# Optimization experiments

Hardware: AMD Instinct MI355X
Metric: run time of the kernel (lower is better)

Reference implementation:

```python
import jax, jax.numpy as jnp
import numpy as np

N_NODES = 100000
N_EDGES = 1600000
IN_C, HID_C, OUT_C = 64, 64, 32


def setup_inputs() -> dict:
    key = jax.random.key(0)
    ks = jax.random.split(key, 6)
    x = jax.random.normal(ks[0], (N_NODES, IN_C), dtype=jnp.float32)
    edge_index = jax.random.randint(ks[1], (2, N_EDGES), 0, N_NODES, dtype=jnp.int64)
    edge_weight = jax.random.uniform(ks[2], (N_EDGES,), dtype=jnp.float32)
    # Glorot-ish init for the two GCNConv weight matrices, zero bias (PyG default)
    W1 = jax.random.normal(ks[3], (IN_C, HID_C), dtype=jnp.float32) / np.sqrt(IN_C)
    b1 = jnp.zeros((HID_C,), dtype=jnp.float32)
    W2 = jax.random.normal(ks[4], (HID_C, OUT_C), dtype=jnp.float32) / np.sqrt(HID_C)
    b2 = jnp.zeros((OUT_C,), dtype=jnp.float32)
    return {"x": x, "edge_index": edge_index, "edge_weight": edge_weight,
            "W1": W1, "b1": b1, "W2": W2, "b2": b2}


def _gcn_conv(x, src, dst, w, W, b):
    """PyG GCNConv: add self-loops (weight 1), symmetric D^-1/2 (A+I) D^-1/2 norm,
    then aggregate transformed features into destination nodes, plus bias."""
    n = x.shape[0]
    loop = jnp.arange(n, dtype=src.dtype)
    s = jnp.concatenate([src, loop])
    d = jnp.concatenate([dst, loop])
    wl = jnp.concatenate([w, jnp.ones((n,), dtype=x.dtype)])
    deg = jax.ops.segment_sum(wl, d, num_segments=n)            # [N]
    dinv = jnp.where(deg > 0, jax.lax.rsqrt(deg), 0.0)
    norm = dinv[s] * wl * dinv[d]                               # [E+N]
    xw = x @ W                                                  # [N, C_out]
    msg = norm[:, None] * xw[s]                                 # gather + scale
    return jax.ops.segment_sum(msg, d, num_segments=n) + b      # scatter-add


def reference(x, edge_index, edge_weight, W1, b1, W2, b2):
    src, dst = edge_index[0], edge_index[1]
    h = _gcn_conv(x, src, dst, edge_weight, W1, b1)
    h = jax.nn.relu(h)
    # dropout(p=0.5, training=self.training): identity in eval mode
    return _gcn_conv(h, src, dst, edge_weight, W2, b2)
```

## Files before the change

kernel.cpp:

```cpp
#include <hip/hip_runtime.h>

#define N_NODES 100000
#define N_EDGES 1600000
#define IN_C 64
#define HID_C 64
#define OUT_C 32

#define NB 391
#define BSHIFT 8
#define BMASK 255
#define SEG_CAP 4864
#define EPB 4096
#define BIN_BLOCKS ((N_EDGES + EPB - 1) / EPB)
#define SMASK 0x1FFFF
#define FIXSCALE 34359738368.0f

__device__ __forceinline__ unsigned int bpack(float a, float b) {
    unsigned int ua = __float_as_uint(a);
    ua += 0x7FFFu + ((ua >> 16) & 1u);
    unsigned int ub = __float_as_uint(b);
    ub += 0x7FFFu + ((ub >> 16) & 1u);
    return (ua >> 16) | (ub & 0xFFFF0000u);
}
__device__ __forceinline__ float2 bup(unsigned int v) {
    return make_float2(__uint_as_float(v << 16), __uint_as_float(v & 0xFFFF0000u));
}


__global__ void __launch_bounds__(256) bin_kernel(const int* __restrict__ src,
                                                  const int* __restrict__ dst,
                                                  const float* __restrict__ w,
                                                  int* __restrict__ gcnt,
                                                  int2* __restrict__ seg) {
    __shared__ int2 recs[EPB];
    __shared__ int meta[EPB];
    __shared__ int hist[NB];
    __shared__ int gbase[NB];
    int tid = threadIdx.x;
    for (int i = tid; i < NB; i += 256) hist[i] = 0;
    __syncthreads();
    int e0 = blockIdx.x * EPB;
    int n = min(EPB, N_EDGES - e0);
    const int4* src4 = (const int4*)(src + e0);
    const int4* dst4 = (const int4*)(dst + e0);
    const float4* w4 = (const float4*)(w + e0);
    int n4 = n >> 2;
    for (int i = tid; i < n4; i += 256) {
        int4 s = src4[i];
        int4 d = dst4[i];
        float4 ww = w4[i];
        int j = i << 2;
#define BIN_ONE(K, SS, DD, WW)                                             \
        {                                                                  \
            int b = (DD) >> BSHIFT;                                        \
            recs[j + K] = make_int2((SS) | (((DD) & BMASK) << 17),         \
                                    __float_as_int(WW));                   \
            int rank = atomicAdd(&hist[b], 1);                             \
            meta[j + K] = b | (rank << 9);                                 \
        }
        BIN_ONE(0, s.x, d.x, ww.x)
        BIN_ONE(1, s.y, d.y, ww.y)
        BIN_ONE(2, s.z, d.z, ww.z)
        BIN_ONE(3, s.w, d.w, ww.w)
#undef BIN_ONE
    }
    __syncthreads();
    for (int b = tid; b < NB; b += 256) {
        int c = hist[b];
        gbase[b] = c ? atomicAdd(&gcnt[b], c) : 0;
    }
    __syncthreads();
    for (int i = tid; i < n; i += 256) {
        int m = meta[i];
        int b = m & 511, rank = m >> 9;
        int pos = gbase[b] + rank;
        if (pos < SEG_CAP) seg[(size_t)b * SEG_CAP + pos] = recs[i];
    }
}


__global__ void __launch_bounds__(256) bsort_kernel(const int* __restrict__ gcnt,
                                                    const int2* __restrict__ seg,
                                                    int2* __restrict__ seg2,
                                                    float* __restrict__ dinv,
                                                    int2* __restrict__ rowRC) {
    __shared__ int2 recs[SEG_CAP];
    __shared__ unsigned long long packed[256];
    __shared__ int meta[SEG_CAP];
    __shared__ int sarr[256];
    __shared__ int ofs0[256];
    int tid = threadIdx.x, b = blockIdx.x;
    int n = min(gcnt[b], SEG_CAP);
    const int2* sp = seg + (size_t)b * SEG_CAP;
    packed[tid] = 0ULL;
    __syncthreads();
    for (int i = tid; i < n; i += 256) {
        int2 r = sp[i];
        recs[i] = r;
        int dl = (r.x >> 17) & BMASK;
        unsigned long long fixw =
            (unsigned long long)(__int_as_float(r.y) * FIXSCALE);
        unsigned long long old = atomicAdd(&packed[dl], (1ULL << 48) | fixw);
        meta[i] = dl | ((int)(old >> 48) << 8);
    }
    __syncthreads();
    unsigned long long p = packed[tid];
    int myc = (int)(p >> 48);
    float degw = (float)((double)(p & ((1ULL << 48) - 1)) * (1.0 / (double)FIXSCALE));
    int node = (b << BSHIFT) + tid;
    if (node < N_NODES) dinv[node] = rsqrtf(1.0f + degw);
    int padc = (myc + 1) & ~1;
    sarr[tid] = padc;
    __syncthreads();
    for (int off = 1; off < 256; off <<= 1) {
        int tmp = (tid >= off) ? sarr[tid - off] : 0;
        __syncthreads();
        sarr[tid] += tmp;
        __syncthreads();
    }
    int excl = sarr[tid] - padc;
    if (node < N_NODES) rowRC[node] = make_int2(b * SEG_CAP + excl, myc);
    ofs0[tid] = excl;
    __syncthreads();
    int2* op = seg2 + (size_t)b * SEG_CAP;
    for (int i = tid; i < n; i += 256) {
        int m = meta[i];
        int dl = m & BMASK, rank = m >> 8;
        op[ofs0[dl] + rank] = recs[i];
    }
}


__global__ void __launch_bounds__(256) gemm1_kernel(const float* __restrict__ X,
                                                    const float* __restrict__ W,
                                                    const float* __restrict__ dinv,
                                                    unsigned int* __restrict__ XWs,
                                                    int nRows) {
    __shared__ float XsT[64][64];
    __shared__ float Ws[64][64];
    int tid = threadIdx.x;
    {
        const float4* Wv = (const float4*)W;
        float4* Wsv = (float4*)&Ws[0][0];
        for (int i = tid; i < 1024; i += 256) Wsv[i] = Wv[i];
    }
    int row0 = blockIdx.x * 64;
    int rmax = nRows - row0;
    for (int i = tid; i < 64 * 16; i += 256) {
        int r = i & 63, kq = i >> 6;
        float4 v = (r < rmax) ? ((const float4*)(X + (size_t)(row0 + r) * IN_C))[kq]
                              : make_float4(0.f, 0.f, 0.f, 0.f);
        XsT[4 * kq + 0][r] = v.x;
        XsT[4 * kq + 1][r] = v.y;
        XsT[4 * kq + 2][r] = v.z;
        XsT[4 * kq + 3][r] = v.w;
    }
    __syncthreads();
    int tr = tid >> 4, tc = tid & 15;
    float acc[4][4] = {};
    float a[4], bb[4];
#pragma unroll 8
    for (int k = 0; k < 64; ++k) {
        *(float4*)a = *(const float4*)&XsT[k][4 * tr];
        *(float4*)bb = *(const float4*)&Ws[k][4 * tc];
#pragma unroll
        for (int i = 0; i < 4; ++i)
#pragma unroll
            for (int j = 0; j < 4; ++j) acc[i][j] += a[i] * bb[j];
    }
#pragma unroll
    for (int i = 0; i < 4; ++i) {
        int rl = 4 * tr + i;
        if (rl < rmax) {
            int row = row0 + rl;
            float di = dinv[row];
            uint2 o;
            o.x = bpack(acc[i][0] * di, acc[i][1] * di);
            o.y = bpack(acc[i][2] * di, acc[i][3] * di);
            ((uint2*)XWs)[(size_t)row * 16 + tc] = o;
        }
    }
}


__global__ void __launch_bounds__(256) agg1_kernel(const int2* __restrict__ rowRC,
                                                   const int2* __restrict__ seg2,
                                                   const unsigned int* __restrict__ XWs,
                                                   const float* __restrict__ dinv,
                                                   const float* __restrict__ b1,
                                                   unsigned int* __restrict__ Hb) {
    int l32 = threadIdx.x & 31;
    int d = blockIdx.x * 8 + (threadIdx.x >> 5);
    if (d >= N_NODES) return;
    float did = dinv[d];
    float2 bv = ((const float2*)b1)[l32];
    float2 s2 = bup(XWs[(size_t)d * 32 + l32]);
    float ax = bv.x + did * s2.x, ay = bv.y + did * s2.y;
    int2 rc = rowRC[d];
    int nc = rc.y;
    const int2* sp = seg2 + rc.x;
    const int4* sp4 = (const int4*)sp;
    int e = 0;
    for (; e + 8 <= nc; e += 8) {
        int4 q0 = sp4[(e >> 1) + 0], q1 = sp4[(e >> 1) + 1];
        int4 q2 = sp4[(e >> 1) + 2], q3 = sp4[(e >> 1) + 3];
        int s0 = q0.x & SMASK, s1 = q0.z & SMASK, s4 = q1.x & SMASK, s5 = q1.z & SMASK;
        int s6 = q2.x & SMASK, s7 = q2.z & SMASK, s8 = q3.x & SMASK, s9 = q3.z & SMASK;
        unsigned int r0 = XWs[(size_t)s0 * 32 + l32];
        unsigned int r1 = XWs[(size_t)s1 * 32 + l32];
        unsigned int r2 = XWs[(size_t)s4 * 32 + l32];
        unsigned int r3 = XWs[(size_t)s5 * 32 + l32];
        unsigned int r4 = XWs[(size_t)s6 * 32 + l32];
        unsigned int r5 = XWs[(size_t)s7 * 32 + l32];
        unsigned int r6 = XWs[(size_t)s8 * 32 + l32];
        unsigned int r7 = XWs[(size_t)s9 * 32 + l32];
        float c0 = __int_as_float(q0.y) * did, c1 = __int_as_float(q0.w) * did;
        float c2 = __int_as_float(q1.y) * did, c3 = __int_as_float(q1.w) * did;
        float c4 = __int_as_float(q2.y) * did, c5 = __int_as_float(q2.w) * did;
        float c6 = __int_as_float(q3.y) * did, c7 = __int_as_float(q3.w) * did;
        float2 v;
        v = bup(r0); ax += c0 * v.x; ay += c0 * v.y;
        v = bup(r1); ax += c1 * v.x; ay += c1 * v.y;
        v = bup(r2); ax += c2 * v.x; ay += c2 * v.y;
        v = bup(r3); ax += c3 * v.x; ay += c3 * v.y;
        v = bup(r4); ax += c4 * v.x; ay += c4 * v.y;
        v = bup(r5); ax += c5 * v.x; ay += c5 * v.y;
        v = bup(r6); ax += c6 * v.x; ay += c6 * v.y;
        v = bup(r7); ax += c7 * v.x; ay += c7 * v.y;
    }
    for (; e + 2 <= nc; e += 2) {
        int4 q = sp4[e >> 1];
        int s0 = q.x & SMASK, s1 = q.z & SMASK;
        unsigned int r0 = XWs[(size_t)s0 * 32 + l32];
        unsigned int r1 = XWs[(size_t)s1 * 32 + l32];
        float c0 = __int_as_float(q.y) * did, c1 = __int_as_float(q.w) * did;
        float2 v;
        v = bup(r0); ax += c0 * v.x; ay += c0 * v.y;
        v = bup(r1); ax += c1 * v.x; ay += c1 * v.y;
    }
    if (e < nc) {
        int2 p = sp[e];
        int s = p.x & SMASK;
        float c = __int_as_float(p.y) * did;
        float2 v = bup(XWs[(size_t)s * 32 + l32]);
        ax += c * v.x;
        ay += c * v.y;
    }
    Hb[(size_t)d * 32 + l32] = bpack(fmaxf(ax, 0.f), fmaxf(ay, 0.f));
}


__global__ void __launch_bounds__(256) gemm2_kernel(const unsigned int* __restrict__ Hb,
                                                    const float* __restrict__ W,
                                                    const float* __restrict__ dinv,
                                                    unsigned int* __restrict__ HWs,
                                                    int nRows) {
    __shared__ float HsT[64][128];
    __shared__ float Ws[64][32];
    int tid = threadIdx.x;
    {
        const float4* Wv = (const float4*)W;
        float4* Wsv = (float4*)&Ws[0][0];
        for (int i = tid; i < 512; i += 256) Wsv[i] = Wv[i];
    }
    int row0 = blockIdx.x * 128;
    int rmax = nRows - row0;
    for (int i = tid; i < 128 * 8; i += 256) {
        int r = i & 127, kq = i >> 7;
        uint4 v = (r < rmax) ? ((const uint4*)(Hb + (size_t)(row0 + r) * 32))[kq]
                             : make_uint4(0u, 0u, 0u, 0u);
        float2 f;
        f = bup(v.x); HsT[8 * kq + 0][r] = f.x; HsT[8 * kq + 1][r] = f.y;
        f = bup(v.y); HsT[8 * kq + 2][r] = f.x; HsT[8 * kq + 3][r] = f.y;
        f = bup(v.z); HsT[8 * kq + 4][r] = f.x; HsT[8 * kq + 5][r] = f.y;
        f = bup(v.w); HsT[8 * kq + 6][r] = f.x; HsT[8 * kq + 7][r] = f.y;
    }
    __syncthreads();
    int tr = tid >> 3, tc = tid & 7;
    float acc[4][4] = {};
    float a[4], bb[4];
#pragma unroll 8
    for (int k = 0; k < 64; ++k) {
        *(float4*)a = *(const float4*)&HsT[k][4 * tr];
        *(float4*)bb = *(const float4*)&Ws[k][4 * tc];
#pragma unroll
        for (int i = 0; i < 4; ++i)
#pragma unroll
            for (int j = 0; j < 4; ++j) acc[i][j] += a[i] * bb[j];
    }
#pragma unroll
    for (int i = 0; i < 4; ++i) {
        int rl = 4 * tr + i;
        if (rl < rmax) {
            int row = row0 + rl;
            float di = dinv[row];
            uint2 o;
            o.x = bpack(acc[i][0] * di, acc[i][1] * di);
            o.y = bpack(acc[i][2] * di, acc[i][3] * di);
            ((uint2*)HWs)[(size_t)row * 8 + tc] = o;
        }
    }
}


__global__ void __launch_bounds__(256) agg2_kernel(const int2* __restrict__ rowRC,
                                                   const int2* __restrict__ seg2,
                                                   const unsigned int* __restrict__ HWs,
                                                   const float* __restrict__ dinv,
                                                   const float* __restrict__ b2,
                                                   float* __restrict__ out) {
    int l16 = threadIdx.x & 15;
    int d = blockIdx.x * 16 + (threadIdx.x >> 4);
    if (d >= N_NODES) return;
    float did = dinv[d];
    float2 bv = ((const float2*)b2)[l16];
    float2 s2 = bup(HWs[(size_t)d * 16 + l16]);
    float ax = bv.x + did * s2.x, ay = bv.y + did * s2.y;
    int2 rc = rowRC[d];
    int nc = rc.y;
    const int2* sp = seg2 + rc.x;
    const int4* sp4 = (const int4*)sp;
    int e = 0;
    for (; e + 8 <= nc; e += 8) {
        int4 q0 = sp4[(e >> 1) + 0], q1 = sp4[(e >> 1) + 1];
        int4 q2 = sp4[(e >> 1) + 2], q3 = sp4[(e >> 1) + 3];
        int s0 = q0.x & SMASK, s1 = q0.z & SMASK, s4 = q1.x & SMASK, s5 = q1.z & SMASK;
        int s6 = q2.x & SMASK, s7 = q2.z & SMASK, s8 = q3.x & SMASK, s9 = q3.z & SMASK;
        unsigned int r0 = HWs[(size_t)s0 * 16 + l16];
        unsigned int r1 = HWs[(size_t)s1 * 16 + l16];
        unsigned int r2 = HWs[(size_t)s4 * 16 + l16];
        unsigned int r3 = HWs[(size_t)s5 * 16 + l16];
        unsigned int r4 = HWs[(size_t)s6 * 16 + l16];
        unsigned int r5 = HWs[(size_t)s7 * 16 + l16];
        unsigned int r6 = HWs[(size_t)s8 * 16 + l16];
        unsigned int r7 = HWs[(size_t)s9 * 16 + l16];
        float c0 = __int_as_float(q0.y) * did, c1 = __int_as_float(q0.w) * did;
        float c2 = __int_as_float(q1.y) * did, c3 = __int_as_float(q1.w) * did;
        float c4 = __int_as_float(q2.y) * did, c5 = __int_as_float(q2.w) * did;
        float c6 = __int_as_float(q3.y) * did, c7 = __int_as_float(q3.w) * did;
        float2 v;
        v = bup(r0); ax += c0 * v.x; ay += c0 * v.y;
        v = bup(r1); ax += c1 * v.x; ay += c1 * v.y;
        v = bup(r2); ax += c2 * v.x; ay += c2 * v.y;
        v = bup(r3); ax += c3 * v.x; ay += c3 * v.y;
        v = bup(r4); ax += c4 * v.x; ay += c4 * v.y;
        v = bup(r5); ax += c5 * v.x; ay += c5 * v.y;
        v = bup(r6); ax += c6 * v.x; ay += c6 * v.y;
        v = bup(r7); ax += c7 * v.x; ay += c7 * v.y;
    }
    for (; e + 2 <= nc; e += 2) {
        int4 q = sp4[e >> 1];
        int s0 = q.x & SMASK, s1 = q.z & SMASK;
        unsigned int r0 = HWs[(size_t)s0 * 16 + l16];
        unsigned int r1 = HWs[(size_t)s1 * 16 + l16];
        float c0 = __int_as_float(q.y) * did, c1 = __int_as_float(q.w) * did;
        float2 v;
        v = bup(r0); ax += c0 * v.x; ay += c0 * v.y;
        v = bup(r1); ax += c1 * v.x; ay += c1 * v.y;
    }
    if (e < nc) {
        int2 p = sp[e];
        int s = p.x & SMASK;
        float c = __int_as_float(p.y) * did;
        float2 v = bup(HWs[(size_t)s * 16 + l16]);
        ax += c * v.x;
        ay += c * v.y;
    }
    ((float2*)out)[(size_t)d * 16 + l16] = make_float2(ax, ay);
}


extern "C" void kernel_launch(void* const* d_in, const int* in_sizes, int n_in,
                              void* d_out, int out_size, void* d_ws, size_t ws_size,
                              hipStream_t stream) {
    const float* x = (const float*)d_in[0];
    const int* edge_index = (const int*)d_in[1];
    const float* ew = (const float*)d_in[2];
    const float* W1 = (const float*)d_in[3];
    const float* b1 = (const float*)d_in[4];
    const float* W2 = (const float*)d_in[5];
    const float* b2 = (const float*)d_in[6];
    float* out = (float*)d_out;

    const int* src = edge_index;
    const int* dst = edge_index + N_EDGES;

    char* ws = (char*)d_ws;
    size_t off = 0;
    auto carve = [&](size_t bytes) -> void* {
        void* p = ws + off;
        off += (bytes + 255) & ~(size_t)255;
        return p;
    };

    int* gcnt = (int*)carve(NB * 4);
    float* dinv = (float*)carve((size_t)N_NODES * 4);
    int2* rowRC = (int2*)carve((size_t)N_NODES * 8);
    int2* seg = (int2*)carve((size_t)NB * SEG_CAP * 8);
    int2* seg2 = (int2*)carve((size_t)NB * SEG_CAP * 8);
    unsigned int* XWs = (unsigned int*)carve((size_t)N_NODES * 32 * 4);
    unsigned int* Hb = (unsigned int*)carve((size_t)N_NODES * 32 * 4);
    unsigned int* HWs = XWs;

    hipMemsetAsync(gcnt, 0, NB * 4, stream);
    bin_kernel<<<BIN_BLOCKS, 256, 0, stream>>>(src, dst, ew, gcnt, seg);
    bsort_kernel<<<NB, 256, 0, stream>>>(gcnt, seg, seg2, dinv, rowRC);
    gemm1_kernel<<<(N_NODES + 63) / 64, 256, 0, stream>>>(x, W1, dinv, XWs, N_NODES);
    agg1_kernel<<<(N_NODES + 7) / 8, 256, 0, stream>>>(rowRC, seg2, XWs, dinv, b1, Hb);
    gemm2_kernel<<<(N_NODES + 127) / 128, 256, 0, stream>>>(Hb, W2, dinv, HWs, N_NODES);
    agg2_kernel<<<(N_NODES + 15) / 16, 256, 0, stream>>>(rowRC, seg2, HWs, dinv, b2, out);
}
```

Measured before the change: 224.4 us.

## Fuse edge binning with first GEMM and widen aggregation loads per lane

The edge binning kernel and the first feature GEMM now run in one launch as disjoint block ranges sharing a union of shared memory, so the GEMM no longer waits for the degree computation. The dinv source scaling moves into the bucket-sort kernel, which rescales its 256 rows of bf16 XW in place after computing degrees. That adds an extra read-modify-write pass and a second bf16 rounding. Both aggregation kernels now give each lane 4 channels via uint2 loads, halving lanes per node and processing twice as many nodes per block.

```diff
diff --git a/kernel.cpp b/kernel.cpp
--- a/kernel.cpp
+++ b/kernel.cpp
@@ -12,6 +12,7 @@
 #define SEG_CAP 4864
 #define EPB 4096
 #define BIN_BLOCKS ((N_EDGES + EPB - 1) / EPB)
+#define G1_BLOCKS ((N_NODES + 63) / 64)
 #define SMASK 0x1FFFF
 #define FIXSCALE 34359738368.0f
 
@@ -27,54 +28,106 @@
 }
 
 
-__global__ void __launch_bounds__(256) bin_kernel(const int* __restrict__ src,
-                                                  const int* __restrict__ dst,
-                                                  const float* __restrict__ w,
-                                                  int* __restrict__ gcnt,
-                                                  int2* __restrict__ seg) {
-    __shared__ int2 recs[EPB];
-    __shared__ int meta[EPB];
-    __shared__ int hist[NB];
-    __shared__ int gbase[NB];
+struct BinSh {
+    int2 recs[EPB];
+    int meta[EPB];
+    int hist[NB];
+    int gbase[NB];
+};
+struct G1Sh {
+    float XsT[64][64];
+    float Ws[64][64];
+};
+union FusedSh { BinSh b; G1Sh g; };
+
+__global__ void __launch_bounds__(256) fused1_kernel(
+    const int* __restrict__ src, const int* __restrict__ dst,
+    const float* __restrict__ w, int* __restrict__ gcnt, int2* __restrict__ seg,
+    const float* __restrict__ X, const float* __restrict__ W,
+    unsigned int* __restrict__ XWu) {
+    __shared__ FusedSh sh;
     int tid = threadIdx.x;
-    for (int i = tid; i < NB; i += 256) hist[i] = 0;
-    __syncthreads();
-    int e0 = blockIdx.x * EPB;
-    int n = min(EPB, N_EDGES - e0);
-    const int4* src4 = (const int4*)(src + e0);
-    const int4* dst4 = (const int4*)(dst + e0);
-    const float4* w4 = (const float4*)(w + e0);
-    int n4 = n >> 2;
-    for (int i = tid; i < n4; i += 256) {
-        int4 s = src4[i];
-        int4 d = dst4[i];
-        float4 ww = w4[i];
-        int j = i << 2;
+    if (blockIdx.x < BIN_BLOCKS) {
+        for (int i = tid; i < NB; i += 256) sh.b.hist[i] = 0;
+        __syncthreads();
+        int e0 = blockIdx.x * EPB;
+        int n = min(EPB, N_EDGES - e0);
+        const int4* src4 = (const int4*)(src + e0);
+        const int4* dst4 = (const int4*)(dst + e0);
+        const float4* w4 = (const float4*)(w + e0);
+        int n4 = n >> 2;
+        for (int i = tid; i < n4; i += 256) {
+            int4 s = src4[i];
+            int4 d = dst4[i];
+            float4 ww = w4[i];
+            int j = i << 2;
 #define BIN_ONE(K, SS, DD, WW)                                             \
-        {                                                                  \
-            int b = (DD) >> BSHIFT;                                        \
-            recs[j + K] = make_int2((SS) | (((DD) & BMASK) << 17),         \
-                                    __float_as_int(WW));                   \
-            int rank = atomicAdd(&hist[b], 1);                             \
-            meta[j + K] = b | (rank << 9);                                 \
-        }
-        BIN_ONE(0, s.x, d.x, ww.x)
-        BIN_ONE(1, s.y, d.y, ww.y)
-        BIN_ONE(2, s.z, d.z, ww.z)
-        BIN_ONE(3, s.w, d.w, ww.w)
+            {                                                              \
+                int b = (DD) >> BSHIFT;                                    \
+                sh.b.recs[j + K] = make_int2((SS) | (((DD) & BMASK) << 17),\
+                                             __float_as_int(WW));          \
+                int rank = atomicAdd(&sh.b.hist[b], 1);                    \
+                sh.b.meta[j + K] = b | (rank << 9);                        \
+            }
+            BIN_ONE(0, s.x, d.x, ww.x)
+            BIN_ONE(1, s.y, d.y, ww.y)
+            BIN_ONE(2, s.z, d.z, ww.z)
+            BIN_ONE(3, s.w, d.w, ww.w)
 #undef BIN_ONE
-    }
-    __syncthreads();
-    for (int b = tid; b < NB; b += 256) {
-        int c = hist[b];
-        gbase[b] = c ? atomicAdd(&gcnt[b], c) : 0;
-    }
-    __syncthreads();
-    for (int i = tid; i < n; i += 256) {
-        int m = meta[i];
-        int b = m & 511, rank = m >> 9;
-        int pos = gbase[b] + rank;
-        if (pos < SEG_CAP) seg[(size_t)b * SEG_CAP + pos] = recs[i];
+        }
+        __syncthreads();
+        for (int b = tid; b < NB; b += 256) {
+            int c = sh.b.hist[b];
+            sh.b.gbase[b] = c ? atomicAdd(&gcnt[b], c) : 0;
+        }
+        __syncthreads();
+        for (int i = tid; i < n; i += 256) {
+            int m = sh.b.meta[i];
+            int b = m & 511, rank = m >> 9;
+            int pos = sh.b.gbase[b] + rank;
+            if (pos < SEG_CAP) seg[(size_t)b * SEG_CAP + pos] = sh.b.recs[i];
+        }
+    } else {
+        {
+            const float4* Wv = (const float4*)W;
+            float4* Wsv = (float4*)&sh.g.Ws[0][0];
+            for (int i = tid; i < 1024; i += 256) Wsv[i] = Wv[i];
+        }
+        int row0 = (blockIdx.x - BIN_BLOCKS) * 64;
+        int rmax = N_NODES - row0;
+        for (int i = tid; i < 64 * 16; i += 256) {
+            int r = i & 63, kq = i >> 6;
+            float4 v = (r < rmax) ? ((const float4*)(X + (size_t)(row0 + r) * IN_C))[kq]
+                                  : make_float4(0.f, 0.f, 0.f, 0.f);
+            sh.g.XsT[4 * kq + 0][r] = v.x;
+            sh.g.XsT[4 * kq + 1][r] = v.y;
+            sh.g.XsT[4 * kq + 2][r] = v.z;
+            sh.g.XsT[4 * kq + 3][r] = v.w;
+        }
+        __syncthreads();
+        int tr = tid >> 4, tc = tid & 15;
+        float acc[4][4] = {};
+        float a[4], bb[4];
+#pragma unroll 8
+        for (int k = 0; k < 64; ++k) {
+            *(float4*)a = *(const float4*)&sh.g.XsT[k][4 * tr];
+            *(float4*)bb = *(const float4*)&sh.g.Ws[k][4 * tc];
+#pragma unroll
+            for (int i = 0; i < 4; ++i)
+#pragma unroll
+                for (int j = 0; j < 4; ++j) acc[i][j] += a[i] * bb[j];
+        }
+#pragma unroll
+        for (int i = 0; i < 4; ++i) {
+            int rl = 4 * tr + i;
+            if (rl < rmax) {
+                int row = row0 + rl;
+                uint2 o;
+                o.x = bpack(acc[i][0], acc[i][1]);
+                o.y = bpack(acc[i][2], acc[i][3]);
+                ((uint2*)XWu)[(size_t)row * 16 + tc] = o;
+            }
+        }
     }
 }
 
@@ -83,12 +136,14 @@
                                                     const int2* __restrict__ seg,
                                                     int2* __restrict__ seg2,
                                                     float* __restrict__ dinv,
-                                                    int2* __restrict__ rowRC) {
+                                                    int2* __restrict__ rowRC,
+                                                    unsigned int* __restrict__ XWs) {
     __shared__ int2 recs[SEG_CAP];
     __shared__ unsigned long long packed[256];
     __shared__ int meta[SEG_CAP];
     __shared__ int sarr[256];
     __shared__ int ofs0[256];
+    __shared__ float dinvsh[256];
     int tid = threadIdx.x, b = blockIdx.x;
     int n = min(gcnt[b], SEG_CAP);
     const int2* sp = seg + (size_t)b * SEG_CAP;
@@ -107,8 +162,10 @@
     unsigned long long p = packed[tid];
     int myc = (int)(p >> 48);
     float degw = (float)((double)(p & ((1ULL << 48) - 1)) * (1.0 / (double)FIXSCALE));
+    float dv = rsqrtf(1.0f + degw);
+    dinvsh[tid] = dv;
     int node = (b << BSHIFT) + tid;
-    if (node < N_NODES) dinv[node] = rsqrtf(1.0f + degw);
+    if (node < N_NODES) dinv[node] = dv;
     int padc = (myc + 1) & ~1;
     sarr[tid] = padc;
     __syncthreads();
@@ -128,57 +185,19 @@
         int dl = m & BMASK, rank = m >> 8;
         op[ofs0[dl] + rank] = recs[i];
     }
-}
-
-
-__global__ void __launch_bounds__(256) gemm1_kernel(const float* __restrict__ X,
-                                                    const float* __restrict__ W,
-                                                    const float* __restrict__ dinv,
-                                                    unsigned int* __restrict__ XWs,
-                                                    int nRows) {
-    __shared__ float XsT[64][64];
-    __shared__ float Ws[64][64];
-    int tid = threadIdx.x;
-    {
-        const float4* Wv = (const float4*)W;
-        float4* Wsv = (float4*)&Ws[0][0];
-        for (int i = tid; i < 1024; i += 256) Wsv[i] = Wv[i];
-    }
-    int row0 = blockIdx.x * 64;
-    int rmax = nRows - row0;
-    for (int i = tid; i < 64 * 16; i += 256) {
-        int r = i & 63, kq = i >> 6;
-        float4 v = (r < rmax) ? ((const float4*)(X + (size_t)(row0 + r) * IN_C))[kq]
-                              : make_float4(0.f, 0.f, 0.f, 0.f);
-        XsT[4 * kq + 0][r] = v.x;
-        XsT[4 * kq + 1][r] = v.y;
-        XsT[4 * kq + 2][r] = v.z;
-        XsT[4 * kq + 3][r] = v.w;
-    }
-    __syncthreads();
-    int tr = tid >> 4, tc = tid & 15;
-    float acc[4][4] = {};
-    float a[4], bb[4];
-#pragma unroll 8
-    for (int k = 0; k < 64; ++k) {
-        *(float4*)a = *(const float4*)&XsT[k][4 * tr];
-        *(float4*)bb = *(const float4*)&Ws[k][4 * tc];
-#pragma unroll
-        for (int i = 0; i < 4; ++i)
-#pragma unroll
-            for (int j = 0; j < 4; ++j) acc[i][j] += a[i] * bb[j];
-    }
-#pragma unroll
-    for (int i = 0; i < 4; ++i) {
-        int rl = 4 * tr + i;
-        if (rl < rmax) {
-            int row = row0 + rl;
-            float di = dinv[row];
-            uint2 o;
-            o.x = bpack(acc[i][0] * di, acc[i][1] * di);
-            o.y = bpack(acc[i][2] * di, acc[i][3] * di);
-            ((uint2*)XWs)[(size_t)row * 16 + tc] = o;
-        }
+    int baseRow = b << BSHIFT;
+    int rowsHere = min(256, N_NODES - baseRow);
+    uint4* XW4 = (uint4*)XWs;
+    for (int i = tid; i < rowsHere * 8; i += 256) {
+        int nl = i >> 3;
+        float s = dinvsh[nl];
+        uint4 v = XW4[(size_t)(baseRow + nl) * 8 + (i & 7)];
+        float2 f;
+        f = bup(v.x); v.x = bpack(f.x * s, f.y * s);
+        f = bup(v.y); v.y = bpack(f.x * s, f.y * s);
+        f = bup(v.z); v.z = bpack(f.x * s, f.y * s);
+        f = bup(v.w); v.w = bpack(f.x * s, f.y * s);
+        XW4[(size_t)(baseRow + nl) * 8 + (i & 7)] = v;
     }
 }
 
@@ -189,13 +208,16 @@
                                                    const float* __restrict__ dinv,
                                                    const float* __restrict__ b1,
                                                    unsigned int* __restrict__ Hb) {
-    int l32 = threadIdx.x & 31;
-    int d = blockIdx.x * 8 + (threadIdx.x >> 5);
+    int l16 = threadIdx.x & 15;
+    int d = blockIdx.x * 16 + (threadIdx.x >> 4);
     if (d >= N_NODES) return;
+    const uint2* XW2 = (const uint2*)XWs;
     float did = dinv[d];
-    float2 bv = ((const float2*)b1)[l32];
-    float2 s2 = bup(XWs[(size_t)d * 32 + l32]);
-    float ax = bv.x + did * s2.x, ay = bv.y + did * s2.y;
+    float4 bv = ((const float4*)b1)[l16];
+    uint2 sv = XW2[(size_t)d * 16 + l16];
+    float2 f0 = bup(sv.x), f1 = bup(sv.y);
+    float a0 = bv.x + did * f0.x, a1 = bv.y + did * f0.y;
+    float a2 = bv.z + did * f1.x, a3 = bv.w + did * f1.y;
     int2 rc = rowRC[d];
     int nc = rc.y;
     const int2* sp = seg2 + rc.x;
@@ -204,49 +226,49 @@
     for (; e + 8 <= nc; e += 8) {
         int4 q0 = sp4[(e >> 1) + 0], q1 = sp4[(e >> 1) + 1];
         int4 q2 = sp4[(e >> 1) + 2], q3 = sp4[(e >> 1) + 3];
-        int s0 = q0.x & SMASK, s1 = q0.z & SMASK, s4 = q1.x & SMASK, s5 = q1.z & SMASK;
-        int s6 = q2.x & SMASK, s7 = q2.z & SMASK, s8 = q3.x & SMASK, s9 = q3.z & SMASK;
-        unsigned int r0 = XWs[(size_t)s0 * 32 + l32];
-        unsigned int r1 = XWs[(size_t)s1 * 32 + l32];
-        unsigned int r2 = XWs[(size_t)s4 * 32 + l32];
-        unsigned int r3 = XWs[(size_t)s5 * 32 + l32];
-        unsigned int r4 = XWs[(size_t)s6 * 32 + l32];
-        unsigned int r5 = XWs[(size_t)s7 * 32 + l32];
-        unsigned int r6 = XWs[(size_t)s8 * 32 + l32];
-        unsigned int r7 = XWs[(size_t)s9 * 32 + l32];
+        int s0 = q0.x & SMASK, s1 = q0.z & SMASK, s2 = q1.x & SMASK, s3 = q1.z & SMASK;
+        int s4 = q2.x & SMASK, s5 = q2.z & SMASK, s6 = q3.x & SMASK, s7 = q3.z & SMASK;
+        uint2 r0 = XW2[(size_t)s0 * 16 + l16];
+        uint2 r1 = XW2[(size_t)s1 * 16 + l16];
+        uint2 r2 = XW2[(size_t)s2 * 16 + l16];
+        uint2 r3 = XW2[(size_t)s3 * 16 + l16];
+        uint2 r4 = XW2[(size_t)s4 * 16 + l16];
+        uint2 r5 = XW2[(size_t)s5 * 16 + l16];
+        uint2 r6 = XW2[(size_t)s6 * 16 + l16];
+        uint2 r7 = XW2[(size_t)s7 * 16 + l16];
         float c0 = __int_as_float(q0.y) * did, c1 = __int_as_float(q0.w) * did;
         float c2 = __int_as_float(q1.y) * did, c3 = __int_as_float(q1.w) * did;
         float c4 = __int_as_float(q2.y) * did, c5 = __int_as_float(q2.w) * did;
         float c6 = __int_as_float(q3.y) * did, c7 = __int_as_float(q3.w) * did;
         float2 v;
-        v = bup(r0); ax += c0 * v.x; ay += c0 * v.y;
-        v = bup(r1); ax += c1 * v.x; ay += c1 * v.y;
-        v = bup(r2); ax += c2 * v.x; ay += c2 * v.y;
-        v = bup(r3); ax += c3 * v.x; ay += c3 * v.y;
-        v = bup(r4); ax += c4 * v.x; ay += c4 * v.y;
-        v = bup(r5); ax += c5 * v.x; ay += c5 * v.y;
-        v = bup(r6); ax += c6 * v.x; ay += c6 * v.y;
-        v = bup(r7); ax += c7 * v.x; ay += c7 * v.y;
+#define ACC1(R, C)                                                         \
+        v = bup(R.x); a0 += (C) * v.x; a1 += (C) * v.y;                    \
+        v = bup(R.y); a2 += (C) * v.x; a3 += (C) * v.y;
+        ACC1(r0, c0) ACC1(r1, c1) ACC1(r2, c2) ACC1(r3, c3)
+        ACC1(r4, c4) ACC1(r5, c5) ACC1(r6, c6) ACC1(r7, c7)
     }
     for (; e + 2 <= nc; e += 2) {
         int4 q = sp4[e >> 1];
         int s0 = q.x & SMASK, s1 = q.z & SMASK;
-        unsigned int r0 = XWs[(size_t)s0 * 32 + l32];
-        unsigned int r1 = XWs[(size_t)s1 * 32 + l32];
+        uint2 r0 = XW2[(size_t)s0 * 16 + l16];
+        uint2 r1 = XW2[(size_t)s1 * 16 + l16];
         float c0 = __int_as_float(q.y) * did, c1 = __int_as_float(q.w) * did;
         float2 v;
-        v = bup(r0); ax += c0 * v.x; ay += c0 * v.y;
-        v = bup(r1); ax += c1 * v.x; ay += c1 * v.y;
+        ACC1(r0, c0) ACC1(r1, c1)
     }
     if (e < nc) {
         int2 p = sp[e];
         int s = p.x & SMASK;
         float c = __int_as_float(p.y) * did;
-        float2 v = bup(XWs[(size_t)s * 32 + l32]);
-        ax += c * v.x;
-        ay += c * v.y;
-    }
-    Hb[(size_t)d * 32 + l32] = bpack(fmaxf(ax, 0.f), fmaxf(ay, 0.f));
+        uint2 r = XW2[(size_t)s * 16 + l16];
+        float2 v;
+        ACC1(r, c)
+    }
+#undef ACC1
+    uint2 o;
+    o.x = bpack(fmaxf(a0, 0.f), fmaxf(a1, 0.f));
+    o.y = bpack(fmaxf(a2, 0.f), fmaxf(a3, 0.f));
+    ((uint2*)Hb)[(size_t)d * 16 + l16] = o;
 }
 
 
@@ -309,13 +331,16 @@
                                                    const float* __restrict__ dinv,
                                                    const float* __restrict__ b2,
                                                    float* __restrict__ out) {
-    int l16 = threadIdx.x & 15;
-    int d = blockIdx.x * 16 + (threadIdx.x >> 4);
+    int l8 = threadIdx.x & 7;
+    int d = blockIdx.x * 32 + (threadIdx.x >> 3);
     if (d >= N_NODES) return;
+    const uint2* HW2 = (const uint2*)HWs;
     float did = dinv[d];
-    float2 bv = ((const float2*)b2)[l16];
-    float2 s2 = bup(HWs[(size_t)d * 16 + l16]);
-    float ax = bv.x + did * s2.x, ay = bv.y + did * s2.y;
+    float4 bv = ((const float4*)b2)[l8];
+    uint2 sv = HW2[(size_t)d * 8 + l8];
+    float2 f0 = bup(sv.x), f1 = bup(sv.y);
+    float a0 = bv.x + did * f0.x, a1 = bv.y + did * f0.y;
+    float a2 = bv.z + did * f1.x, a3 = bv.w + did * f1.y;
     int2 rc = rowRC[d];
     int nc = rc.y;
     const int2* sp = seg2 + rc.x;
@@ -324,49 +349,46 @@
     for (; e + 8 <= nc; e += 8) {
         int4 q0 = sp4[(e >> 1) + 0], q1 = sp4[(e >> 1) + 1];
         int4 q2 = sp4[(e >> 1) + 2], q3 = sp4[(e >> 1) + 3];
-        int s0 = q0.x & SMASK, s1 = q0.z & SMASK, s4 = q1.x & SMASK, s5 = q1.z & SMASK;
-        int s6 = q2.x & SMASK, s7 = q2.z & SMASK, s8 = q3.x & SMASK, s9 = q3.z & SMASK;
-        unsigned int r0 = HWs[(size_t)s0 * 16 + l16];
-        unsigned int r1 = HWs[(size_t)s1 * 16 + l16];
-        unsigned int r2 = HWs[(size_t)s4 * 16 + l16];
-        unsigned int r3 = HWs[(size_t)s5 * 16 + l16];
-        unsigned int r4 = HWs[(size_t)s6 * 16 + l16];
-        unsigned int r5 = HWs[(size_t)s7 * 16 + l16];
-        unsigned int r6 = HWs[(size_t)s8 * 16 + l16];
-        unsigned int r7 = HWs[(size_t)s9 * 16 + l16];
+        int s0 = q0.x & SMASK, s1 = q0.z & SMASK, s2 = q1.x & SMASK, s3 = q1.z & SMASK;
+        int s4 = q2.x & SMASK, s5 = q2.z & SMASK, s6 = q3.x & SMASK, s7 = q3.z & SMASK;
+        uint2 r0 = HW2[(size_t)s0 * 8 + l8];
+        uint2 r1 = HW2[(size_t)s1 * 8 + l8];
+        uint2 r2 = HW2[(size_t)s2 * 8 + l8];
+        uint2 r3 = HW2[(size_t)s3 * 8 + l8];
+        uint2 r4 = HW2[(size_t)s4 * 8 + l8];
+        uint2 r5 = HW2[(size_t)s5 * 8 + l8];
+        uint2 r6 = HW2[(size_t)s6 * 8 + l8];
+        uint2 r7 = HW2[(size_t)s7 * 8 + l8];
         float c0 = __int_as_float(q0.y) * did, c1 = __int_as_float(q0.w) * did;
         float c2 = __int_as_float(q1.y) * did, c3 = __int_as_float(q1.w) * did;
         float c4 = __int_as_float(q2.y) * did, c5 = __int_as_float(q2.w) * did;
         float c6 = __int_as_float(q3.y) * did, c7 = __int_as_float(q3.w) * did;
         float2 v;
-        v = bup(r0); ax += c0 * v.x; ay += c0 * v.y;
-        v = bup(r1); ax += c1 * v.x; ay += c1 * v.y;
-        v = bup(r2); ax += c2 * v.x; ay += c2 * v.y;
-        v = bup(r3); ax += c3 * v.x; ay += c3 * v.y;
-        v = bup(r4); ax += c4 * v.x; ay += c4 * v.y;
-        v = bup(r5); ax += c5 * v.x; ay += c5 * v.y;
-        v = bup(r6); ax += c6 * v.x; ay += c6 * v.y;
-        v = bup(r7); ax += c7 * v.x; ay += c7 * v.y;
+#define ACC2(R, C)                                                         \
+        v = bup(R.x); a0 += (C) * v.x; a1 += (C) * v.y;                    \
+        v = bup(R.y); a2 += (C) * v.x; a3 += (C) * v.y;
+        ACC2(r0, c0) ACC2(r1, c1) ACC2(r2, c2) ACC2(r3, c3)
+        ACC2(r4, c4) ACC2(r5, c5) ACC2(r6, c6) ACC2(r7, c7)
     }
     for (; e + 2 <= nc; e += 2) {
         int4 q = sp4[e >> 1];
         int s0 = q.x & SMASK, s1 = q.z & SMASK;
-        unsigned int r0 = HWs[(size_t)s0 * 16 + l16];
-        unsigned int r1 = HWs[(size_t)s1 * 16 + l16];
+        uint2 r0 = HW2[(size_t)s0 * 8 + l8];
+        uint2 r1 = HW2[(size_t)s1 * 8 + l8];
         float c0 = __int_as_float(q.y) * did, c1 = __int_as_float(q.w) * did;
         float2 v;
-        v = bup(r0); ax += c0 * v.x; ay += c0 * v.y;
-        v = bup(r1); ax += c1 * v.x; ay += c1 * v.y;
+        ACC2(r0, c0) ACC2(r1, c1)
     }
     if (e < nc) {
         int2 p = sp[e];
         int s = p.x & SMASK;
         float c = __int_as_float(p.y) * did;
-        float2 v = bup(HWs[(size_t)s * 16 + l16]);
-        ax += c * v.x;
-        ay += c * v.y;
-    }
-    ((float2*)out)[(size_t)d * 16 + l16] = make_float2(ax, ay);
+        uint2 r = HW2[(size_t)s * 8 + l8];
+        float2 v;
+        ACC2(r, c)
+    }
+#undef ACC2
+    ((float4*)out)[(size_t)d * 8 + l8] = make_float4(a0, a1, a2, a3);
 }
 
 
@@ -403,10 +425,10 @@
     unsigned int* HWs = XWs;
 
     hipMemsetAsync(gcnt, 0, NB * 4, stream);
-    bin_kernel<<<BIN_BLOCKS, 256, 0, stream>>>(src, dst, ew, gcnt, seg);
-    bsort_kernel<<<NB, 256, 0, stream>>>(gcnt, seg, seg2, dinv, rowRC);
-    gemm1_kernel<<<(N_NODES + 63) / 64, 256, 0, stream>>>(x, W1, dinv, XWs, N_NODES);
-    agg1_kernel<<<(N_NODES + 7) / 8, 256, 0, stream>>>(rowRC, seg2, XWs, dinv, b1, Hb);
+    fused1_kernel<<<BIN_BLOCKS + G1_BLOCKS, 256, 0, stream>>>(src, dst, ew, gcnt, seg,
+                                                              x, W1, XWs);
+    bsort_kernel<<<NB, 256, 0, stream>>>(gcnt, seg, seg2, dinv, rowRC, XWs);
+    agg1_kernel<<<(N_NODES + 15) / 16, 256, 0, stream>>>(rowRC, seg2, XWs, dinv, b1, Hb);
     gemm2_kernel<<<(N_NODES + 127) / 128, 256, 0, stream>>>(Hb, W2, dinv, HWs, N_NODES);
-    agg2_kernel<<<(N_NODES + 15) / 16, 256, 0, stream>>>(rowRC, seg2, HWs, dinv, b2, out);
-}
+    agg2_kernel<<<(N_NODES + 31) / 32, 256, 0, stream>>>(rowRC, seg2, HWs, dinv, b2, out);
+}
```

After: 222.5 us. No clear change (-0.8%).
